# Kernel tuning notes

Hardware: AMD Instinct MI355X
Metric: run time of the kernel (lower is better)

The kernel has to match this reference:

```python
import jax, jax.numpy as jnp
import numpy as np

B, N, H, NH = 1024, 101, 128, 8
HD = H // NH
EPS = 1e-5  # torch LayerNorm default


def _xavier(k, shape):
    fan_in, fan_out = shape
    lim = float(np.sqrt(6.0 / (fan_in + fan_out)))
    return jax.random.uniform(k, shape, jnp.float32, -lim, lim)


def setup_inputs() -> dict:
    key = jax.random.key(0)
    ks = jax.random.split(key, 12)
    return {
        "encoder_inputs": jax.random.normal(ks[0], (B, N, H), jnp.float32),
        "pool": jax.random.normal(ks[1], (B, H), jnp.float32),
        "capacity": jnp.ones((B, 1), jnp.float32),
        "demand": jax.random.uniform(ks[2], (B, N), jnp.float32),
        "fc_w": _xavier(ks[3], (H + 1, H)),      # nn.Linear(hidden+1, hidden, bias=False), stored [in,out]
        "fc1_w": _xavier(ks[4], (H, H)),
        "dec_ln_g": jnp.ones((H,), jnp.float32),
        "dec_ln_b": jnp.zeros((H,), jnp.float32),
        "wq": _xavier(ks[5], (H, H)),             # TransformerAttention q/k/v/out projections
        "wk": _xavier(ks[6], (H, H)),
        "wv": _xavier(ks[7], (H, H)),
        "wo": _xavier(ks[8], (H, H)),
        "kp_w": _xavier(ks[9], (H, H)),           # pointer self.k
        "ptr_ln_g": jnp.ones((H,), jnp.float32),
        "ptr_ln_b": jnp.zeros((H,), jnp.float32),
        "n_steps": 120,
        "T": 1,
        "greedy": 1,
    }


def _ln(x, g, b):
    mu = x.mean(-1, keepdims=True)
    v = ((x - mu) ** 2).mean(-1, keepdims=True)
    return (x - mu) * jax.lax.rsqrt(v + EPS) * g + b


def _forward(encoder_inputs, pool, capacity, demand, fc_w, fc1_w, dec_ln_g, dec_ln_b,
             wq, wk, wv, wo, kp_w, ptr_ln_g, ptr_ln_b, n_steps, T):
    b, n, h = encoder_inputs.shape
    # context projections are loop-invariant -> hoist out of the decode loop
    Kh = (encoder_inputs @ wk).reshape(b, n, NH, HD)
    Vh = (encoder_inputs @ wv).reshape(b, n, NH, HD)
    Kp = encoder_inputs @ kp_w            # [B,N,H] pointer keys
    pool_proc = pool @ fc1_w              # [B,H]
    ar = jnp.arange(n)
    arB = jnp.arange(b)
    inv_sqrt_hd = 1.0 / jnp.sqrt(jnp.float32(HD))
    inv_sqrt_h = 1.0 / jnp.sqrt(jnp.float32(h))

    def step(carry, i):
        mask1, cap, idx, inp = carry
        # decoder input: fc([emb, remaining_cap]) + fc1(pool), LayerNorm
        d = jnp.concatenate([inp, cap], -1) @ fc_w + pool_proc
        d = _ln(d, dec_ln_g, dec_ln_b)
        # ---- update_mask ----
        hit = (ar[None, :] == idx[:, None]) & (idx[:, None] != 0)
        mask1 = jnp.where((i > 0) & hit, 1.0, mask1)
        infeas = (mask1[:, 1:] > 0) | (demand[:, 1:] > cap)      # customers
        any_feas = jnp.any(~infeas, axis=-1)
        depot_m = jnp.where(i == 0, True, (idx == 0) & any_feas)  # mask depot if at depot & feasible cust exists
        all_cust = jnp.all(infeas, axis=-1)
        depot_m = jnp.where(all_cust, False, depot_m)             # only depot allowed if no feasible customer
        mb = jnp.concatenate([depot_m[:, None], infeas], axis=1)  # [B,N] bool, True = masked
        # ---- TransformerAttention (mhalayer) ----
        Qh = (d @ wq).reshape(b, NH, HD)
        logit = jnp.einsum('bhd,bnhd->bhn', Qh, Kh) * inv_sqrt_hd
        logit = jnp.where(mb[:, None, :], -jnp.inf, logit)
        attn = jax.nn.softmax(logit, axis=-1)
        x = jnp.einsum('bhn,bnhd->bhd', attn, Vh).reshape(b, h) @ wo
        # ---- pointer compatibility ----
        xn = _ln(x, ptr_ln_g, ptr_ln_b)
        comp = jnp.einsum('bh,bnh->bn', xn, Kp) * inv_sqrt_h
        comp = jnp.where(mb, -jnp.inf, comp)
        comp = jnp.where(jnp.all(mb, axis=-1, keepdims=True), 0.0, comp)
        p = jax.nn.softmax(comp / T, axis=-1) + 1e-10
        p = p / p.sum(axis=-1, keepdims=True)
        idx = jnp.argmax(p, axis=-1)                              # greedy selection
        lp = jnp.log(jnp.take_along_axis(p, idx[:, None], 1)[:, 0])
        done = mask1[:, 1:].sum(-1) >= (n - 1)
        lp = jnp.where(done, 0.0, lp)
        # ---- update_state (demand lookups via .item() in torch -> stop_gradient) ----
        sel = jax.lax.stop_gradient(jnp.take_along_axis(demand, idx[:, None], 1))
        cap = jnp.where(idx[:, None] == 0, jax.lax.stop_gradient(capacity), cap - sel)
        inp = encoder_inputs[arB, idx]
        return (mask1, cap, idx, inp), (idx, lp)

    init = (jnp.zeros((b, n), jnp.float32), capacity,
            jnp.zeros((b,), jnp.int32), encoder_inputs[:, 0])
    _, (idxs, lps) = jax.lax.scan(step, init, jnp.arange(n_steps))
    last = idxs[-1]
    final = jnp.where(last == 0, -1, 0).astype(jnp.int32)
    actions = jnp.concatenate(
        [jnp.zeros((b, 1), jnp.int32), idxs.T.astype(jnp.int32), final[:, None]], axis=1)
    log_p = lps.sum(0)
    return actions, log_p


def reference(encoder_inputs, pool, capacity, demand, fc_w, fc1_w, dec_ln_g, dec_ln_b,
              wq, wk, wv, wo, kp_w, ptr_ln_g, ptr_ln_b, n_steps, T, greedy):
    # greedy flag: this reference implements the greedy=True path (deterministic argmax).
    return _forward(encoder_inputs, pool, capacity, demand, fc_w, fc1_w, dec_ln_g,
                    dec_ln_b, wq, wk, wv, wo, kp_w, ptr_ln_g, ptr_ln_b,
                    int(n_steps), float(T))
```

## Files before the change

kernel.cpp:

```cpp
#include <hip/hip_runtime.h>
#include <math.h>

constexpr int N_ = 101, H_ = 128;
constexpr float EPS_ = 1e-5f;

constexpr int OFF_QEF = 0;
constexpr int OFF_KT  = 12928;
constexpr int OFF_AT  = 25960;
constexpr int OFF_XV  = 26776;
constexpr int OFF_YR  = 26920;
constexpr int OFF_CP  = 27064;
constexpr int OFF_RS  = 27192;
constexpr int LDS_WORDS = 27512;
constexpr int LDS_BYTES = LDS_WORDS * 4;

__device__ __forceinline__ float rdlane(float v, int l) {
  return __int_as_float(__builtin_amdgcn_readlane(__float_as_int(v), l));
}
template<int CTRL, int RM>
__device__ __forceinline__ float dppadd(float x) {
  int v = __builtin_amdgcn_update_dpp(0, __float_as_int(x), CTRL, RM, 0xf, true);
  return x + __int_as_float(v);
}
template<int CTRL, int RM>
__device__ __forceinline__ float dppmax(float x) {
  int v = __builtin_amdgcn_update_dpp(__float_as_int(x), __float_as_int(x), CTRL, RM, 0xf, false);
  return fmaxf(x, __int_as_float(v));
}
__device__ __forceinline__ float wave_sum(float x) {
  x = dppadd<0x111,0xf>(x); x = dppadd<0x112,0xf>(x);
  x = dppadd<0x114,0xf>(x); x = dppadd<0x118,0xf>(x);
  x = dppadd<0x142,0xa>(x); x = dppadd<0x143,0xc>(x);
  return rdlane(x, 63);
}
__device__ __forceinline__ float wave_max(float x) {
  x = dppmax<0x111,0xf>(x); x = dppmax<0x112,0xf>(x);
  x = dppmax<0x114,0xf>(x); x = dppmax<0x118,0xf>(x);
  x = dppmax<0x142,0xa>(x); x = dppmax<0x143,0xc>(x);
  return rdlane(x, 63);
}
__device__ __forceinline__ float grp4_sum(float x) {
  x = dppadd<0x111,0xf>(x);
  x = dppadd<0x112,0xf>(x);
  return x;
}
__device__ __forceinline__ int swz(int k) { return (k >> 5) * 36 + (k & 31); }

__global__ __launch_bounds__(512, 2) void gat_decoder(
    const float* __restrict__ enc, const float* __restrict__ pool,
    const float* __restrict__ capac, const float* __restrict__ dem,
    const float* __restrict__ fcw, const float* __restrict__ fc1w,
    const float* __restrict__ lng, const float* __restrict__ lnb,
    const float* __restrict__ wq, const float* __restrict__ wk,
    const float* __restrict__ wvm, const float* __restrict__ wo,
    const float* __restrict__ kpw, const float* __restrict__ plg,
    const float* __restrict__ plb, const int* __restrict__ tp,
    float* __restrict__ out, int Bv, int ns)
{
  extern __shared__ float sm[];
  const int tid  = threadIdx.x;
  const int b    = blockIdx.x;
  const int lane = tid & 63;
  const int wvid = tid >> 6;
  const int sl   = lane & 3;
  const int lc   = lane >> 2;
  const int col  = wvid * 16 + lc;
  const int n1 = lane, n2 = lane + 64;

  const float NEG_INF = -__builtin_inff();
  int ti = tp[0];
  float Tf = (ti > 1000000 || ti < -1000000) ? __int_as_float((int)ti) : (float)ti;
  const float inv_sqrt_h = 1.0f / sqrtf(128.0f);
  const float PSUM_CONST = 1.0f + (float)N_ * 1e-10f;

  const float* encb = enc + (size_t)b * (N_ * H_);

  float* QEF = sm + OFF_QEF; float* KT = sm + OFF_KT;
  float* AT = sm + OFF_AT;   float* XVp = sm + OFF_XV;
  float* YRp = sm + OFF_YR;  float* CP = sm + OFF_CP;
  float* RS = sm + OFF_RS;

  const int j3 = tid & 127;
  const int g3 = __builtin_amdgcn_readfirstlane(tid >> 7);
  const int r03 = g3 * 26, nr3 = (g3 == 3) ? 23 : 26;

  {
    const float* pb = pool + (size_t)b * H_;
    float p = 0.f;
    #pragma unroll
    for (int r = 0; r < 32; ++r) p = fmaf(pb[g3 * 32 + r], fc1w[(g3 * 32 + r) * H_ + j3], p);
    AT[g3 * 128 + j3] = p;
  }
  {
    float acc[26];
    #pragma unroll
    for (int t = 0; t < 26; ++t) acc[t] = 0.f;
    for (int k0 = 0; k0 < H_; k0 += 8) {
      float w8[8];
      #pragma unroll
      for (int kk = 0; kk < 8; ++kk) w8[kk] = kpw[(k0 + kk) * H_ + j3];
      #pragma unroll
      for (int t = 0; t < 26; ++t) if (t < nr3) {
        const float* ep = encb + (r03 + t) * H_ + k0;
        #pragma unroll
        for (int kk = 0; kk < 8; ++kk) acc[t] = fmaf(ep[kk], w8[kk], acc[t]);
      }
    }
    #pragma unroll
    for (int t = 0; t < 26; ++t) if (t < nr3) KT[(r03 + t) * 129 + j3] = acc[t];
  }
  __syncthreads();

  if (tid < 128) CP[tid] = AT[tid] + AT[128 + tid] + AT[256 + tid] + AT[384 + tid];
  float kpT[32], kps, cpb;
  {
    const int neff = (col < N_) ? col : (N_ - 1);
    const float* src = KT + neff * 129 + sl * 32;
    float ks = 0.f, cb = 0.f;
    #pragma unroll
    for (int r = 0; r < 32; ++r) {
      const float kv = src[r];
      const float pg = plg[sl * 32 + r];
      const float pb2 = plb[sl * 32 + r];
      ks = fmaf(kv, pg, ks);
      cb = fmaf(kv, pb2, cb);
      kpT[r] = kv * pg;
    }
    kps = grp4_sum(ks); cpb = grp4_sum(cb);
  }
  __syncthreads();

  {
    const float pcj = CP[j3];
    float acc[26];
    #pragma unroll
    for (int t = 0; t < 26; ++t) acc[t] = pcj;
    for (int k0 = 0; k0 < H_; k0 += 8) {
      float w8[8];
      #pragma unroll
      for (int kk = 0; kk < 8; ++kk) w8[kk] = fcw[(k0 + kk) * H_ + j3];
      #pragma unroll
      for (int t = 0; t < 26; ++t) if (t < nr3) {
        const float* ep = encb + (r03 + t) * H_ + k0;
        #pragma unroll
        for (int kk = 0; kk < 8; ++kk) acc[t] = fmaf(ep[kk], w8[kk], acc[t]);
      }
    }
    #pragma unroll
    for (int t = 0; t < 26; ++t) if (t < nr3) KT[(r03 + t) * 129 + j3] = acc[t];
  }
  __syncthreads();

  {
    float qacc[26];
    #pragma unroll
    for (int t = 0; t < 26; ++t) qacc[t] = 0.f;
    for (int k0 = 0; k0 < H_; k0 += 8) {
      float w8[8];
      #pragma unroll
      for (int kk = 0; kk < 8; ++kk) w8[kk] = wq[(k0 + kk) * H_ + j3] * lng[k0 + kk];
      #pragma unroll
      for (int t = 0; t < 26; ++t) if (t < nr3) {
        const float* erow = KT + (r03 + t) * 129 + k0;
        #pragma unroll
        for (int kk = 0; kk < 8; ++kk) qacc[t] = fmaf(erow[kk], w8[kk], qacc[t]);
      }
    }
    #pragma unroll
    for (int t = 0; t < 26; ++t) if (t < nr3) QEF[(r03 + t) * 128 + j3] = qacc[t];
  }
  if (tid < N_) {
    const float* base = KT + tid * 129;
    float s = 0.f, s2 = 0.f, sf = 0.f, fs = 0.f, fs2 = 0.f;
    for (int r = 0; r < 128; ++r) {
      const float v = base[r];
      const float fr = fcw[128 * H_ + r];
      s += v; s2 = fmaf(v, v, s2); sf = fmaf(v, fr, sf);
      fs += fr; fs2 = fmaf(fr, fr, fs2);
    }
    RS[tid] = s; RS[104 + tid] = s2; RS[208 + tid] = sf;
    if (tid == 0) { RS[312] = fs; RS[313] = fs2; }
  }
  __syncthreads();

  {
    float acc[26];
    #pragma unroll
    for (int t = 0; t < 26; ++t) acc[t] = 0.f;
    for (int k0 = 0; k0 < H_; k0 += 8) {
      float w8[8];
      #pragma unroll
      for (int kk = 0; kk < 8; ++kk) w8[kk] = wk[(k0 + kk) * H_ + j3];
      #pragma unroll
      for (int t = 0; t < 26; ++t) if (t < nr3) {
        const float* ep = encb + (r03 + t) * H_ + k0;
        #pragma unroll
        for (int kk = 0; kk < 8; ++kk) acc[t] = fmaf(ep[kk], w8[kk], acc[t]);
      }
    }
    #pragma unroll
    for (int t = 0; t < 26; ++t) if (t < nr3) KT[(r03 + t) * 129 + j3] = acc[t];
  }
  float vh[26];
  {
    const int r0v = sl * 26, nrv = (sl == 3) ? 23 : 26;
    #pragma unroll
    for (int t = 0; t < 26; ++t) vh[t] = 0.f;
    for (int k0 = 0; k0 < H_; k0 += 8) {
      float w8[8];
      #pragma unroll
      for (int kk = 0; kk < 8; ++kk) w8[kk] = wvm[(k0 + kk) * H_ + col];
      #pragma unroll
      for (int t = 0; t < 26; ++t) if (t < nrv) {
        const float* ep = encb + (r0v + t) * H_ + k0;
        #pragma unroll
        for (int kk = 0; kk < 8; ++kk) vh[t] = fmaf(ep[kk], w8[kk], vh[t]);
      }
    }
  }
  float wo_r[32];
  #pragma unroll
  for (int r = 0; r < 32; ++r) wo_r[r] = wo[(sl * 32 + r) * H_ + col];
  float wqs = 0.f, qb = 0.f, wfc = 0.f;
  for (int r = 0; r < 128; ++r) {
    const float w = wq[r * H_ + col];
    const float lg = lng[r], lb = lnb[r], fr = fcw[128 * H_ + r];
    wqs = fmaf(w, lg, wqs);
    qb  = fmaf(w, lb, qb);
    wfc = fmaf(w * lg, fr, wfc);
  }
  const float capv = capac[b];
  float cap = capv, lpsum = 0.f;
  float demA = dem[(size_t)b * N_ + n1];
  float demC = (n2 < N_) ? dem[(size_t)b * N_ + n2] : 0.f;
  int vis = 0, pidx = 0;
  bool m1a = false, m1c = false, mbA, mbB;
  {
    bool infA = (n1 >= 1) && (demA > cap);
    bool infB = (n2 >= N_) || (demC > cap);
    bool feasA = (n1 >= 1) && !infA;
    bool feasB = (n2 < N_) && !infB;
    const bool anyf = __any(feasA || feasB);
    mbA = (n1 == 0) ? anyf : infA;
    mbB = infB;
  }
  __syncthreads();
  const float fcsum = RS[312], fcs2 = RS[313];

  for (int i = 0; i < ns; ++i) {
    const int pu = __builtin_amdgcn_readfirstlane(pidx);

    {
      const float efsum = RS[pu], efs2 = RS[104 + pu], effc = RS[208 + pu];
      const float mu = (efsum + cap * fcsum) * (1.f / 128.f);
      const float msq = (efs2 + 2.f * cap * effc + cap * cap * fcs2) * (1.f / 128.f);
      const float inv = 1.0f / sqrtf(msq - mu * mu + EPS_);
      const float qefv = QEF[pu * 128 + col];
      const float q = inv * (qefv + cap * wfc - mu * wqs) + qb;
      const float* kb1 = KT + n1 * 129 + wvid * 16;
      const float* kb2 = KT + ((n2 < N_) ? n2 : n1) * 129 + wvid * 16;
      float a1 = 0.f, a2r = 0.f;
      #pragma unroll
      for (int d = 0; d < 16; ++d) {
        const float qdv = rdlane(q, 4 * d);
        a1  = fmaf(qdv, kb1[d], a1);
        a2r = fmaf(qdv, kb2[d], a2r);
      }
      a1 = mbA ? NEG_INF : a1 * 0.25f;
      float a2 = (n2 < N_ && !mbB) ? a2r * 0.25f : NEG_INF;
      const float mx = wave_max(fmaxf(a1, a2));
      float e1 = expf(a1 - mx);
      float e2 = (n2 < N_) ? expf(a2 - mx) : 0.f;
      const float ss = wave_sum(e1 + e2);
      AT[wvid * N_ + n1] = e1 / ss;
      if (n2 < N_) AT[wvid * N_ + n2] = e2 / ss;
      const float* aw = AT + wvid * N_ + sl * 26;
      const int nrv = (sl == 3) ? 23 : 26;
      float x = 0.f;
      #pragma unroll
      for (int t = 0; t < 26; ++t) if (t < nrv) x = fmaf(aw[t], vh[t], x);
      x = grp4_sum(x);
      if (sl == 3) XVp[swz(col)] = x;
    }
    __syncthreads();

    {
      const float4* xp4 = (const float4*)(XVp + sl * 36);
      float y = 0.f;
      #pragma unroll
      for (int r4 = 0; r4 < 8; ++r4) {
        const float4 u = xp4[r4];
        y = fmaf(wo_r[r4 * 4 + 0], u.x, y);
        y = fmaf(wo_r[r4 * 4 + 1], u.y, y);
        y = fmaf(wo_r[r4 * 4 + 2], u.z, y);
        y = fmaf(wo_r[r4 * 4 + 3], u.w, y);
      }
      y = grp4_sum(y);
      if (sl == 3) YRp[swz(col)] = y;
    }
    __syncthreads();

    {
      const float YA = YRp[swz(n1)], YC = YRp[swz(n2 & 127)];
      const float mu = wave_sum(YA + YC) * (1.f / 128.f);
      const float da = YA - mu, dc = YC - mu;
      const float inv = 1.0f / sqrtf(wave_sum(da * da + dc * dc) * (1.f / 128.f) + EPS_);
      const float4* yp4 = (const float4*)(YRp + sl * 36);
      float c = 0.f;
      #pragma unroll
      for (int r4 = 0; r4 < 8; ++r4) {
        const float4 u = yp4[r4];
        c = fmaf(kpT[r4 * 4 + 0], u.x, c);
        c = fmaf(kpT[r4 * 4 + 1], u.y, c);
        c = fmaf(kpT[r4 * 4 + 2], u.z, c);
        c = fmaf(kpT[r4 * 4 + 3], u.w, c);
      }
      c = grp4_sum(c);
      const float comp = inv * (c - mu * kps) + cpb;
      if (sl == 3 && col < N_) CP[col] = comp;
    }
    __syncthreads();

    {
      const bool allmb = __all(mbA && mbB);
      float c1 = mbA ? NEG_INF : CP[n1] * inv_sqrt_h / Tf;
      float c2 = (n2 < N_ && !mbB) ? CP[n2 & 127] * inv_sqrt_h / Tf : NEG_INF;
      if (allmb) { c1 = 0.f; c2 = (n2 < N_) ? 0.f : NEG_INF; }
      const float mx = wave_max(fmaxf(c1, c2));
      const unsigned long long b1 = __ballot(c1 == mx);
      const unsigned long long b2 = __ballot(c2 == mx);
      const int bis = b1 ? (__ffsll((long long)b1) - 1)
                         : (64 + __ffsll((long long)b2) - 1);
      float e1 = expf(c1 - mx);
      float e2 = (n2 < N_) ? expf(c2 - mx) : 0.f;
      const float ss = wave_sum(e1 + e2);
      float lp = logf((1.0f / ss + 1e-10f) / PSUM_CONST);
      if (vis >= N_ - 1) lp = 0.f;
      lpsum += lp;
      const float dsel = (bis < 64) ? rdlane(demA, bis) : rdlane(demC, bis - 64);
      cap = (bis == 0) ? capv : (cap - dsel);
      if (bis != 0) {
        const bool newly = ((bis == n1) && !m1a) || ((bis == n2) && !m1c);
        if (__any(newly)) vis += 1;
        m1a = m1a || (bis == n1);
        m1c = m1c || (bis == n2);
      }
      bool infA = (n1 >= 1) && (m1a || demA > cap);
      bool infB = (n2 >= N_) || m1c || (demC > cap);
      bool feasA = (n1 >= 1) && !infA;
      bool feasB = (n2 < N_) && !infB;
      const bool anyf = __any(feasA || feasB);
      const bool depot_m = anyf && (bis == 0);
      mbA = (n1 == 0) ? depot_m : infA;
      mbB = infB;
      pidx = bis;
      if (wvid == 0 && lane == 0) out[(size_t)b * (ns + 2) + 1 + i] = (float)bis;
    }
  }

  if (wvid == 0 && lane == 0) {
    out[(size_t)b * (ns + 2)] = 0.f;
    out[(size_t)b * (ns + 2) + ns + 1] = (pidx == 0) ? -1.f : 0.f;
    out[(size_t)Bv * (ns + 2) + b] = lpsum;
  }
}

extern "C" void kernel_launch(void* const* d_in, const int* in_sizes, int n_in,
                              void* d_out, int out_size, void* d_ws, size_t ws_size,
                              hipStream_t stream) {
  const int Bv = in_sizes[0] / (N_ * H_);
  const int ns = out_size / Bv - 3;
  (void)hipFuncSetAttribute(reinterpret_cast<const void*>(gat_decoder),
                            hipFuncAttributeMaxDynamicSharedMemorySize, LDS_BYTES);
  gat_decoder<<<dim3(Bv), dim3(512), LDS_BYTES, stream>>>(
      (const float*)d_in[0],  (const float*)d_in[1],  (const float*)d_in[2],
      (const float*)d_in[3],  (const float*)d_in[4],  (const float*)d_in[5],
      (const float*)d_in[6],  (const float*)d_in[7],  (const float*)d_in[8],
      (const float*)d_in[9],  (const float*)d_in[10], (const float*)d_in[11],
      (const float*)d_in[12], (const float*)d_in[13], (const float*)d_in[14],
      (const int*)d_in[16],
      (float*)d_out, Bv, ns);
}
```

Measured before the change: 2.911 ms.

## Hold attention keys in registers and share one LDS table to double occupancy

Attention key heads, previously stored in LDS, are now loaded once into per-thread registers (khA/khB) and used from there in the decode loop. The QEF and KT regions are merged into one reused LDS table, with the precompute phases reordered so that table is free in time. That roughly halves LDS use, and the launch bound is raised to 4 blocks per CU with static shared memory. The goal is more resident blocks and no per-step LDS key reads, at the cost of 32 extra registers per thread under a tighter register budget, which may cause spilling.

```diff
diff --git a/kernel.cpp b/kernel.cpp
--- a/kernel.cpp
+++ b/kernel.cpp
@@ -4,15 +4,13 @@
 constexpr int N_ = 101, H_ = 128;
 constexpr float EPS_ = 1e-5f;
 
-constexpr int OFF_QEF = 0;
-constexpr int OFF_KT  = 12928;
-constexpr int OFF_AT  = 25960;
-constexpr int OFF_XV  = 26776;
-constexpr int OFF_YR  = 26920;
-constexpr int OFF_CP  = 27064;
-constexpr int OFF_RS  = 27192;
-constexpr int LDS_WORDS = 27512;
-constexpr int LDS_BYTES = LDS_WORDS * 4;
+constexpr int OFF_TAB = 0;
+constexpr int OFF_AT  = 13032;
+constexpr int OFF_XV  = OFF_AT + 816;
+constexpr int OFF_YR  = OFF_XV + 144;
+constexpr int OFF_CP  = OFF_YR + 144;
+constexpr int OFF_RS  = OFF_CP + 128;
+constexpr int LDS_WORDS = OFF_RS + 320;
 
 __device__ __forceinline__ float rdlane(float v, int l) {
   return __int_as_float(__builtin_amdgcn_readlane(__float_as_int(v), l));
@@ -46,7 +44,7 @@
 }
 __device__ __forceinline__ int swz(int k) { return (k >> 5) * 36 + (k & 31); }
 
-__global__ __launch_bounds__(512, 2) void gat_decoder(
+__global__ __launch_bounds__(512, 4) void gat_decoder(
     const float* __restrict__ enc, const float* __restrict__ pool,
     const float* __restrict__ capac, const float* __restrict__ dem,
     const float* __restrict__ fcw, const float* __restrict__ fc1w,
@@ -57,7 +55,7 @@
     const float* __restrict__ plb, const int* __restrict__ tp,
     float* __restrict__ out, int Bv, int ns)
 {
-  extern __shared__ float sm[];
+  __shared__ float sm[LDS_WORDS];
   const int tid  = threadIdx.x;
   const int b    = blockIdx.x;
   const int lane = tid & 63;
@@ -75,7 +73,7 @@
 
   const float* encb = enc + (size_t)b * (N_ * H_);
 
-  float* QEF = sm + OFF_QEF; float* KT = sm + OFF_KT;
+  float* TAB = sm + OFF_TAB;
   float* AT = sm + OFF_AT;   float* XVp = sm + OFF_XV;
   float* YRp = sm + OFF_YR;  float* CP = sm + OFF_CP;
   float* RS = sm + OFF_RS;
@@ -107,7 +105,7 @@
       }
     }
     #pragma unroll
-    for (int t = 0; t < 26; ++t) if (t < nr3) KT[(r03 + t) * 129 + j3] = acc[t];
+    for (int t = 0; t < 26; ++t) if (t < nr3) TAB[(r03 + t) * 129 + j3] = acc[t];
   }
   __syncthreads();
 
@@ -115,7 +113,7 @@
   float kpT[32], kps, cpb;
   {
     const int neff = (col < N_) ? col : (N_ - 1);
-    const float* src = KT + neff * 129 + sl * 32;
+    const float* src = TAB + neff * 129 + sl * 32;
     float ks = 0.f, cb = 0.f;
     #pragma unroll
     for (int r = 0; r < 32; ++r) {
@@ -131,6 +129,36 @@
   __syncthreads();
 
   {
+    float acc[26];
+    #pragma unroll
+    for (int t = 0; t < 26; ++t) acc[t] = 0.f;
+    for (int k0 = 0; k0 < H_; k0 += 8) {
+      float w8[8];
+      #pragma unroll
+      for (int kk = 0; kk < 8; ++kk) w8[kk] = wk[(k0 + kk) * H_ + j3];
+      #pragma unroll
+      for (int t = 0; t < 26; ++t) if (t < nr3) {
+        const float* ep = encb + (r03 + t) * H_ + k0;
+        #pragma unroll
+        for (int kk = 0; kk < 8; ++kk) acc[t] = fmaf(ep[kk], w8[kk], acc[t]);
+      }
+    }
+    #pragma unroll
+    for (int t = 0; t < 26; ++t) if (t < nr3) TAB[(r03 + t) * 129 + j3] = acc[t];
+  }
+  __syncthreads();
+
+  float khA[16], khB[16];
+  {
+    const int row2 = (n2 < N_) ? n2 : n1;
+    const float* s1 = TAB + n1 * 129 + wvid * 16;
+    const float* s2 = TAB + row2 * 129 + wvid * 16;
+    #pragma unroll
+    for (int d = 0; d < 16; ++d) { khA[d] = s1[d]; khB[d] = s2[d]; }
+  }
+  __syncthreads();
+
+  {
     const float pcj = CP[j3];
     float acc[26];
     #pragma unroll
@@ -147,30 +175,12 @@
       }
     }
     #pragma unroll
-    for (int t = 0; t < 26; ++t) if (t < nr3) KT[(r03 + t) * 129 + j3] = acc[t];
-  }
-  __syncthreads();
-
-  {
-    float qacc[26];
-    #pragma unroll
-    for (int t = 0; t < 26; ++t) qacc[t] = 0.f;
-    for (int k0 = 0; k0 < H_; k0 += 8) {
-      float w8[8];
-      #pragma unroll
-      for (int kk = 0; kk < 8; ++kk) w8[kk] = wq[(k0 + kk) * H_ + j3] * lng[k0 + kk];
-      #pragma unroll
-      for (int t = 0; t < 26; ++t) if (t < nr3) {
-        const float* erow = KT + (r03 + t) * 129 + k0;
-        #pragma unroll
-        for (int kk = 0; kk < 8; ++kk) qacc[t] = fmaf(erow[kk], w8[kk], qacc[t]);
-      }
-    }
-    #pragma unroll
-    for (int t = 0; t < 26; ++t) if (t < nr3) QEF[(r03 + t) * 128 + j3] = qacc[t];
-  }
+    for (int t = 0; t < 26; ++t) if (t < nr3) TAB[(r03 + t) * 129 + j3] = acc[t];
+  }
+  __syncthreads();
+
   if (tid < N_) {
-    const float* base = KT + tid * 129;
+    const float* base = TAB + tid * 129;
     float s = 0.f, s2 = 0.f, sf = 0.f, fs = 0.f, fs2 = 0.f;
     for (int r = 0; r < 128; ++r) {
       const float v = base[r];
@@ -181,26 +191,26 @@
     RS[tid] = s; RS[104 + tid] = s2; RS[208 + tid] = sf;
     if (tid == 0) { RS[312] = fs; RS[313] = fs2; }
   }
-  __syncthreads();
-
-  {
-    float acc[26];
-    #pragma unroll
-    for (int t = 0; t < 26; ++t) acc[t] = 0.f;
-    for (int k0 = 0; k0 < H_; k0 += 8) {
-      float w8[8];
-      #pragma unroll
-      for (int kk = 0; kk < 8; ++kk) w8[kk] = wk[(k0 + kk) * H_ + j3];
+  float qacc[26];
+  {
+    #pragma unroll
+    for (int t = 0; t < 26; ++t) qacc[t] = 0.f;
+    for (int k0 = 0; k0 < H_; k0 += 8) {
+      float w8[8];
+      #pragma unroll
+      for (int kk = 0; kk < 8; ++kk) w8[kk] = wq[(k0 + kk) * H_ + j3] * lng[k0 + kk];
       #pragma unroll
       for (int t = 0; t < 26; ++t) if (t < nr3) {
-        const float* ep = encb + (r03 + t) * H_ + k0;
-        #pragma unroll
-        for (int kk = 0; kk < 8; ++kk) acc[t] = fmaf(ep[kk], w8[kk], acc[t]);
-      }
-    }
-    #pragma unroll
-    for (int t = 0; t < 26; ++t) if (t < nr3) KT[(r03 + t) * 129 + j3] = acc[t];
-  }
+        const float* erow = TAB + (r03 + t) * 129 + k0;
+        #pragma unroll
+        for (int kk = 0; kk < 8; ++kk) qacc[t] = fmaf(erow[kk], w8[kk], qacc[t]);
+      }
+    }
+  }
+  __syncthreads();
+
+  #pragma unroll
+  for (int t = 0; t < 26; ++t) if (t < nr3) TAB[(r03 + t) * 128 + j3] = qacc[t];
   float vh[26];
   {
     const int r0v = sl * 26, nrv = (sl == 3) ? 23 : 26;
@@ -255,16 +265,14 @@
       const float mu = (efsum + cap * fcsum) * (1.f / 128.f);
       const float msq = (efs2 + 2.f * cap * effc + cap * cap * fcs2) * (1.f / 128.f);
       const float inv = 1.0f / sqrtf(msq - mu * mu + EPS_);
-      const float qefv = QEF[pu * 128 + col];
+      const float qefv = TAB[pu * 128 + col];
       const float q = inv * (qefv + cap * wfc - mu * wqs) + qb;
-      const float* kb1 = KT + n1 * 129 + wvid * 16;
-      const float* kb2 = KT + ((n2 < N_) ? n2 : n1) * 129 + wvid * 16;
       float a1 = 0.f, a2r = 0.f;
       #pragma unroll
       for (int d = 0; d < 16; ++d) {
         const float qdv = rdlane(q, 4 * d);
-        a1  = fmaf(qdv, kb1[d], a1);
-        a2r = fmaf(qdv, kb2[d], a2r);
+        a1  = fmaf(qdv, khA[d], a1);
+        a2r = fmaf(qdv, khB[d], a2r);
       }
       a1 = mbA ? NEG_INF : a1 * 0.25f;
       float a2 = (n2 < N_ && !mbB) ? a2r * 0.25f : NEG_INF;
@@ -370,9 +378,7 @@
                               hipStream_t stream) {
   const int Bv = in_sizes[0] / (N_ * H_);
   const int ns = out_size / Bv - 3;
-  (void)hipFuncSetAttribute(reinterpret_cast<const void*>(gat_decoder),
-                            hipFuncAttributeMaxDynamicSharedMemorySize, LDS_BYTES);
-  gat_decoder<<<dim3(Bv), dim3(512), LDS_BYTES, stream>>>(
+  gat_decoder<<<dim3(Bv), dim3(512), 0, stream>>>(
       (const float*)d_in[0],  (const float*)d_in[1],  (const float*)d_in[2],
       (const float*)d_in[3],  (const float*)d_in[4],  (const float*)d_in[5],
       (const float*)d_in[6],  (const float*)d_in[7],  (const float*)d_in[8],
```

New measurement: 4.856 ms. +66.8%, slower.

## Process two batch elements per workgroup to amortize barriers and weight loads

Applied to the files above, without the earlier changes.

Each 512-thread block now decodes two batch items at once, interleaving their per-step attention, projection and pointer phases so they share one set of barriers and the register-resident weight loads. The attention keys are moved from LDS into registers, and LDS regions are duplicated per item. The block count is halved and launch bounds drop to one block per SIMD group, which raises register pressure and lowers occupancy. The launch also assumes an even batch size.

```diff
diff --git a/kernel.cpp b/kernel.cpp
--- a/kernel.cpp
+++ b/kernel.cpp
@@ -4,14 +4,19 @@
 constexpr int N_ = 101, H_ = 128;
 constexpr float EPS_ = 1e-5f;
 
-constexpr int OFF_QEF = 0;
-constexpr int OFF_KT  = 12928;
-constexpr int OFF_AT  = 25960;
-constexpr int OFF_XV  = 26776;
-constexpr int OFF_YR  = 26920;
-constexpr int OFF_CP  = 27064;
-constexpr int OFF_RS  = 27192;
-constexpr int LDS_WORDS = 27512;
+constexpr int OFF_REGA = 0;
+constexpr int OFF_REGB = 13056;
+constexpr int OFF_ATA  = 26112;
+constexpr int OFF_ATB  = 26928;
+constexpr int OFF_XVA  = 27744;
+constexpr int OFF_XVB  = 27888;
+constexpr int OFF_YRA  = 28032;
+constexpr int OFF_YRB  = 28176;
+constexpr int OFF_CPA  = 28320;
+constexpr int OFF_CPB  = 28448;
+constexpr int OFF_RSA  = 28576;
+constexpr int OFF_RSB  = 28896;
+constexpr int LDS_WORDS = 29216;
 constexpr int LDS_BYTES = LDS_WORDS * 4;
 
 __device__ __forceinline__ float rdlane(float v, int l) {
@@ -46,7 +51,68 @@
 }
 __device__ __forceinline__ int swz(int k) { return (k >> 5) * 36 + (k & 31); }
 
-__global__ __launch_bounds__(512, 2) void gat_decoder(
+__device__ __forceinline__ void stage_tab(const float* __restrict__ W,
+                                          const float* __restrict__ ENCB,
+                                          float* __restrict__ REG,
+                                          int j3, int r03, int nr3, float init)
+{
+  float acc[26];
+  #pragma unroll
+  for (int t = 0; t < 26; ++t) acc[t] = init;
+  for (int k0 = 0; k0 < H_; k0 += 8) {
+    float w8[8];
+    #pragma unroll
+    for (int kk = 0; kk < 8; ++kk) w8[kk] = W[(k0 + kk) * H_ + j3];
+    #pragma unroll
+    for (int t = 0; t < 26; ++t) if (t < nr3) {
+      const float* ep = ENCB + (r03 + t) * H_ + k0;
+      #pragma unroll
+      for (int kk = 0; kk < 8; ++kk) acc[t] = fmaf(ep[kk], w8[kk], acc[t]);
+    }
+  }
+  #pragma unroll
+  for (int t = 0; t < 26; ++t) if (t < nr3) REG[(r03 + t) * 129 + j3] = acc[t];
+}
+
+__device__ __forceinline__ void row_stats(const float* __restrict__ REG,
+                                          float* __restrict__ RS,
+                                          const float* __restrict__ fcw, int tid)
+{
+  if (tid < N_) {
+    const float* base = REG + tid * 129;
+    float s = 0.f, s2 = 0.f, sf = 0.f, fs = 0.f, fs2 = 0.f;
+    for (int r = 0; r < 128; ++r) {
+      const float v = base[r];
+      const float fr = fcw[128 * H_ + r];
+      s += v; s2 = fmaf(v, v, s2); sf = fmaf(v, fr, sf);
+      fs += fr; fs2 = fmaf(fr, fr, fs2);
+    }
+    RS[tid] = s; RS[104 + tid] = s2; RS[208 + tid] = sf;
+    if (tid == 0) { RS[312] = fs; RS[313] = fs2; }
+  }
+}
+
+__device__ __forceinline__ void qef_compute(const float* __restrict__ REG,
+                                            const float* __restrict__ wq,
+                                            const float* __restrict__ lng,
+                                            int j3, int r03, int nr3, float (&qacc)[26])
+{
+  #pragma unroll
+  for (int t = 0; t < 26; ++t) qacc[t] = 0.f;
+  for (int k0 = 0; k0 < H_; k0 += 8) {
+    float w8[8];
+    #pragma unroll
+    for (int kk = 0; kk < 8; ++kk) w8[kk] = wq[(k0 + kk) * H_ + j3] * lng[k0 + kk];
+    #pragma unroll
+    for (int t = 0; t < 26; ++t) if (t < nr3) {
+      const float* erow = REG + (r03 + t) * 129 + k0;
+      #pragma unroll
+      for (int kk = 0; kk < 8; ++kk) qacc[t] = fmaf(erow[kk], w8[kk], qacc[t]);
+    }
+  }
+}
+
+__global__ __launch_bounds__(512, 1) void gat_decoder(
     const float* __restrict__ enc, const float* __restrict__ pool,
     const float* __restrict__ capac, const float* __restrict__ dem,
     const float* __restrict__ fcw, const float* __restrict__ fc1w,
@@ -59,162 +125,134 @@
 {
   extern __shared__ float sm[];
   const int tid  = threadIdx.x;
-  const int b    = blockIdx.x;
   const int lane = tid & 63;
   const int wvid = tid >> 6;
   const int sl   = lane & 3;
   const int lc   = lane >> 2;
   const int col  = wvid * 16 + lc;
   const int n1 = lane, n2 = lane + 64;
+  const int b0 = blockIdx.x * 2, b1 = b0 + 1;
 
   const float NEG_INF = -__builtin_inff();
   int ti = tp[0];
   float Tf = (ti > 1000000 || ti < -1000000) ? __int_as_float((int)ti) : (float)ti;
   const float inv_sqrt_h = 1.0f / sqrtf(128.0f);
+  const float sT = inv_sqrt_h / Tf;
   const float PSUM_CONST = 1.0f + (float)N_ * 1e-10f;
 
-  const float* encb = enc + (size_t)b * (N_ * H_);
-
-  float* QEF = sm + OFF_QEF; float* KT = sm + OFF_KT;
-  float* AT = sm + OFF_AT;   float* XVp = sm + OFF_XV;
-  float* YRp = sm + OFF_YR;  float* CP = sm + OFF_CP;
-  float* RS = sm + OFF_RS;
+  const float* encA = enc + (size_t)b0 * (N_ * H_);
+  const float* encB = enc + (size_t)b1 * (N_ * H_);
+
+  float* REG_A = sm + OFF_REGA; float* REG_B = sm + OFF_REGB;
+  float* AT_A = sm + OFF_ATA;   float* AT_B = sm + OFF_ATB;
+  float* XV_A = sm + OFF_XVA;   float* XV_B = sm + OFF_XVB;
+  float* YR_A = sm + OFF_YRA;   float* YR_B = sm + OFF_YRB;
+  float* CP_A = sm + OFF_CPA;   float* CP_B = sm + OFF_CPB;
+  float* RS_A = sm + OFF_RSA;   float* RS_B = sm + OFF_RSB;
 
   const int j3 = tid & 127;
   const int g3 = __builtin_amdgcn_readfirstlane(tid >> 7);
   const int r03 = g3 * 26, nr3 = (g3 == 3) ? 23 : 26;
 
   {
-    const float* pb = pool + (size_t)b * H_;
-    float p = 0.f;
-    #pragma unroll
-    for (int r = 0; r < 32; ++r) p = fmaf(pb[g3 * 32 + r], fc1w[(g3 * 32 + r) * H_ + j3], p);
-    AT[g3 * 128 + j3] = p;
-  }
-  {
-    float acc[26];
-    #pragma unroll
-    for (int t = 0; t < 26; ++t) acc[t] = 0.f;
+    const float* pa = pool + (size_t)b0 * H_;
+    const float* pb = pool + (size_t)b1 * H_;
+    float sa = 0.f, sb = 0.f;
+    #pragma unroll
+    for (int r = 0; r < 32; ++r) {
+      const float w = fc1w[(g3 * 32 + r) * H_ + j3];
+      sa = fmaf(pa[g3 * 32 + r], w, sa);
+      sb = fmaf(pb[g3 * 32 + r], w, sb);
+    }
+    AT_A[g3 * 128 + j3] = sa;
+    AT_B[g3 * 128 + j3] = sb;
+  }
+  __syncthreads();
+  if (tid < 128) {
+    CP_A[tid] = AT_A[tid] + AT_A[128 + tid] + AT_A[256 + tid] + AT_A[384 + tid];
+    CP_B[tid] = AT_B[tid] + AT_B[128 + tid] + AT_B[256 + tid] + AT_B[384 + tid];
+  }
+
+  stage_tab(kpw, encA, REG_A, j3, r03, nr3, 0.f);
+  stage_tab(kpw, encB, REG_B, j3, r03, nr3, 0.f);
+  __syncthreads();
+  float kpT_a[32], kps_a, cpb_a, kpT_b[32], kps_b, cpb_b;
+  {
+    const int neff = (col < N_) ? col : (N_ - 1);
+    const float* sa = REG_A + neff * 129 + sl * 32;
+    const float* sb = REG_B + neff * 129 + sl * 32;
+    float ka = 0.f, ca = 0.f, kb = 0.f, cb = 0.f;
+    #pragma unroll
+    for (int r = 0; r < 32; ++r) {
+      const float pg = plg[sl * 32 + r];
+      const float pl = plb[sl * 32 + r];
+      const float va = sa[r], vb = sb[r];
+      ka = fmaf(va, pg, ka); ca = fmaf(va, pl, ca);
+      kb = fmaf(vb, pg, kb); cb = fmaf(vb, pl, cb);
+      kpT_a[r] = va * pg; kpT_b[r] = vb * pg;
+    }
+    kps_a = grp4_sum(ka); cpb_a = grp4_sum(ca);
+    kps_b = grp4_sum(kb); cpb_b = grp4_sum(cb);
+  }
+  __syncthreads();
+
+  stage_tab(wk, encA, REG_A, j3, r03, nr3, 0.f);
+  stage_tab(wk, encB, REG_B, j3, r03, nr3, 0.f);
+  __syncthreads();
+  float khA_a[16], khB_a[16], khA_b[16], khB_b[16];
+  {
+    const int row2 = (n2 < N_) ? n2 : n1;
+    const float* a1p = REG_A + n1 * 129 + wvid * 16;
+    const float* a2p = REG_A + row2 * 129 + wvid * 16;
+    const float* b1p = REG_B + n1 * 129 + wvid * 16;
+    const float* b2p = REG_B + row2 * 129 + wvid * 16;
+    #pragma unroll
+    for (int d = 0; d < 16; ++d) {
+      khA_a[d] = a1p[d]; khB_a[d] = a2p[d];
+      khA_b[d] = b1p[d]; khB_b[d] = b2p[d];
+    }
+  }
+  __syncthreads();
+
+  stage_tab(fcw, encA, REG_A, j3, r03, nr3, CP_A[j3]);
+  stage_tab(fcw, encB, REG_B, j3, r03, nr3, CP_B[j3]);
+  __syncthreads();
+
+  row_stats(REG_A, RS_A, fcw, tid);
+  {
+    float qacc[26];
+    qef_compute(REG_A, wq, lng, j3, r03, nr3, qacc);
+    __syncthreads();
+    #pragma unroll
+    for (int t = 0; t < 26; ++t) if (t < nr3) REG_A[(r03 + t) * 128 + j3] = qacc[t];
+  }
+  row_stats(REG_B, RS_B, fcw, tid);
+  {
+    float qacc[26];
+    qef_compute(REG_B, wq, lng, j3, r03, nr3, qacc);
+    __syncthreads();
+    #pragma unroll
+    for (int t = 0; t < 26; ++t) if (t < nr3) REG_B[(r03 + t) * 128 + j3] = qacc[t];
+  }
+
+  float vh_a[26], vh_b[26];
+  {
+    const int r0v = sl * 26, nrv = (sl == 3) ? 23 : 26;
+    #pragma unroll
+    for (int t = 0; t < 26; ++t) { vh_a[t] = 0.f; vh_b[t] = 0.f; }
     for (int k0 = 0; k0 < H_; k0 += 8) {
       float w8[8];
       #pragma unroll
-      for (int kk = 0; kk < 8; ++kk) w8[kk] = kpw[(k0 + kk) * H_ + j3];
-      #pragma unroll
-      for (int t = 0; t < 26; ++t) if (t < nr3) {
-        const float* ep = encb + (r03 + t) * H_ + k0;
+      for (int kk = 0; kk < 8; ++kk) w8[kk] = wvm[(k0 + kk) * H_ + col];
+      #pragma unroll
+      for (int t = 0; t < 26; ++t) if (t < nrv) {
+        const float* ea = encA + (r0v + t) * H_ + k0;
+        const float* eb = encB + (r0v + t) * H_ + k0;
         #pragma unroll
-        for (int kk = 0; kk < 8; ++kk) acc[t] = fmaf(ep[kk], w8[kk], acc[t]);
-      }
-    }
-    #pragma unroll
-    for (int t = 0; t < 26; ++t) if (t < nr3) KT[(r03 + t) * 129 + j3] = acc[t];
-  }
-  __syncthreads();
-
-  if (tid < 128) CP[tid] = AT[tid] + AT[128 + tid] + AT[256 + tid] + AT[384 + tid];
-  float kpT[32], kps, cpb;
-  {
-    const int neff = (col < N_) ? col : (N_ - 1);
-    const float* src = KT + neff * 129 + sl * 32;
-    float ks = 0.f, cb = 0.f;
-    #pragma unroll
-    for (int r = 0; r < 32; ++r) {
-      const float kv = src[r];
-      const float pg = plg[sl * 32 + r];
-      const float pb2 = plb[sl * 32 + r];
-      ks = fmaf(kv, pg, ks);
-      cb = fmaf(kv, pb2, cb);
-      kpT[r] = kv * pg;
-    }
-    kps = grp4_sum(ks); cpb = grp4_sum(cb);
-  }
-  __syncthreads();
-
-  {
-    const float pcj = CP[j3];
-    float acc[26];
-    #pragma unroll
-    for (int t = 0; t < 26; ++t) acc[t] = pcj;
-    for (int k0 = 0; k0 < H_; k0 += 8) {
-      float w8[8];
-      #pragma unroll
-      for (int kk = 0; kk < 8; ++kk) w8[kk] = fcw[(k0 + kk) * H_ + j3];
-      #pragma unroll
-      for (int t = 0; t < 26; ++t) if (t < nr3) {
-        const float* ep = encb + (r03 + t) * H_ + k0;
-        #pragma unroll
-        for (int kk = 0; kk < 8; ++kk) acc[t] = fmaf(ep[kk], w8[kk], acc[t]);
-      }
-    }
-    #pragma unroll
-    for (int t = 0; t < 26; ++t) if (t < nr3) KT[(r03 + t) * 129 + j3] = acc[t];
-  }
-  __syncthreads();
-
-  {
-    float qacc[26];
-    #pragma unroll
-    for (int t = 0; t < 26; ++t) qacc[t] = 0.f;
-    for (int k0 = 0; k0 < H_; k0 += 8) {
-      float w8[8];
-      #pragma unroll
-      for (int kk = 0; kk < 8; ++kk) w8[kk] = wq[(k0 + kk) * H_ + j3] * lng[k0 + kk];
-      #pragma unroll
-      for (int t = 0; t < 26; ++t) if (t < nr3) {
-        const float* erow = KT + (r03 + t) * 129 + k0;
-        #pragma unroll
-        for (int kk = 0; kk < 8; ++kk) qacc[t] = fmaf(erow[kk], w8[kk], qacc[t]);
-      }
-    }
-    #pragma unroll
-    for (int t = 0; t < 26; ++t) if (t < nr3) QEF[(r03 + t) * 128 + j3] = qacc[t];
-  }
-  if (tid < N_) {
-    const float* base = KT + tid * 129;
-    float s = 0.f, s2 = 0.f, sf = 0.f, fs = 0.f, fs2 = 0.f;
-    for (int r = 0; r < 128; ++r) {
-      const float v = base[r];
-      const float fr = fcw[128 * H_ + r];
-      s += v; s2 = fmaf(v, v, s2); sf = fmaf(v, fr, sf);
-      fs += fr; fs2 = fmaf(fr, fr, fs2);
-    }
-    RS[tid] = s; RS[104 + tid] = s2; RS[208 + tid] = sf;
-    if (tid == 0) { RS[312] = fs; RS[313] = fs2; }
-  }
-  __syncthreads();
-
-  {
-    float acc[26];
-    #pragma unroll
-    for (int t = 0; t < 26; ++t) acc[t] = 0.f;
-    for (int k0 = 0; k0 < H_; k0 += 8) {
-      float w8[8];
-      #pragma unroll
-      for (int kk = 0; kk < 8; ++kk) w8[kk] = wk[(k0 + kk) * H_ + j3];
-      #pragma unroll
-      for (int t = 0; t < 26; ++t) if (t < nr3) {
-        const float* ep = encb + (r03 + t) * H_ + k0;
-        #pragma unroll
-        for (int kk = 0; kk < 8; ++kk) acc[t] = fmaf(ep[kk], w8[kk], acc[t]);
-      }
-    }
-    #pragma unroll
-    for (int t = 0; t < 26; ++t) if (t < nr3) KT[(r03 + t) * 129 + j3] = acc[t];
-  }
-  float vh[26];
-  {
-    const int r0v = sl * 26, nrv = (sl == 3) ? 23 : 26;
-    #pragma unroll
-    for (int t = 0; t < 26; ++t) vh[t] = 0.f;
-    for (int k0 = 0; k0 < H_; k0 += 8) {
-      float w8[8];
-      #pragma unroll
-      for (int kk = 0; kk < 8; ++kk) w8[kk] = wvm[(k0 + kk) * H_ + col];
-      #pragma unroll
-      for (int t = 0; t < 26; ++t) if (t < nrv) {
-        const float* ep = encb + (r0v + t) * H_ + k0;
-        #pragma unroll
-        for (int kk = 0; kk < 8; ++kk) vh[t] = fmaf(ep[kk], w8[kk], vh[t]);
+        for (int kk = 0; kk < 8; ++kk) {
+          vh_a[t] = fmaf(ea[kk], w8[kk], vh_a[t]);
+          vh_b[t] = fmaf(eb[kk], w8[kk], vh_b[t]);
+        }
       }
     }
   }
@@ -229,139 +267,223 @@
     qb  = fmaf(w, lb, qb);
     wfc = fmaf(w * lg, fr, wfc);
   }
-  const float capv = capac[b];
-  float cap = capv, lpsum = 0.f;
-  float demA = dem[(size_t)b * N_ + n1];
-  float demC = (n2 < N_) ? dem[(size_t)b * N_ + n2] : 0.f;
-  int vis = 0, pidx = 0;
-  bool m1a = false, m1c = false, mbA, mbB;
-  {
-    bool infA = (n1 >= 1) && (demA > cap);
-    bool infB = (n2 >= N_) || (demC > cap);
-    bool feasA = (n1 >= 1) && !infA;
-    bool feasB = (n2 < N_) && !infB;
-    const bool anyf = __any(feasA || feasB);
-    mbA = (n1 == 0) ? anyf : infA;
-    mbB = infB;
-  }
-  __syncthreads();
-  const float fcsum = RS[312], fcs2 = RS[313];
+  const float capv_a = capac[b0], capv_b = capac[b1];
+  float cap_a = capv_a, cap_b = capv_b, lpsum_a = 0.f, lpsum_b = 0.f;
+  float demA_a = dem[(size_t)b0 * N_ + n1];
+  float demC_a = (n2 < N_) ? dem[(size_t)b0 * N_ + n2] : 0.f;
+  float demA_b = dem[(size_t)b1 * N_ + n1];
+  float demC_b = (n2 < N_) ? dem[(size_t)b1 * N_ + n2] : 0.f;
+  int vis_a = 0, pidx_a = 0, vis_b = 0, pidx_b = 0;
+  bool m1a_a = false, m1c_a = false, mbA_a, mbB_a;
+  bool m1a_b = false, m1c_b = false, mbA_b, mbB_b;
+  {
+    bool infA = (n1 >= 1) && (demA_a > cap_a);
+    bool infB = (n2 >= N_) || (demC_a > cap_a);
+    const bool anyf = __any(((n1 >= 1) && !infA) || ((n2 < N_) && !infB));
+    mbA_a = (n1 == 0) ? anyf : infA;
+    mbB_a = infB;
+  }
+  {
+    bool infA = (n1 >= 1) && (demA_b > cap_b);
+    bool infB = (n2 >= N_) || (demC_b > cap_b);
+    const bool anyf = __any(((n1 >= 1) && !infA) || ((n2 < N_) && !infB));
+    mbA_b = (n1 == 0) ? anyf : infA;
+    mbB_b = infB;
+  }
+  __syncthreads();
+  const float fcsum = RS_A[312], fcs2 = RS_A[313];
 
   for (int i = 0; i < ns; ++i) {
-    const int pu = __builtin_amdgcn_readfirstlane(pidx);
-
-    {
-      const float efsum = RS[pu], efs2 = RS[104 + pu], effc = RS[208 + pu];
-      const float mu = (efsum + cap * fcsum) * (1.f / 128.f);
-      const float msq = (efs2 + 2.f * cap * effc + cap * cap * fcs2) * (1.f / 128.f);
+    {
+      const int pu = __builtin_amdgcn_readfirstlane(pidx_a);
+      const float efsum = RS_A[pu], efs2 = RS_A[104 + pu], effc = RS_A[208 + pu];
+      const float mu = (efsum + cap_a * fcsum) * (1.f / 128.f);
+      const float msq = (efs2 + 2.f * cap_a * effc + cap_a * cap_a * fcs2) * (1.f / 128.f);
       const float inv = 1.0f / sqrtf(msq - mu * mu + EPS_);
-      const float qefv = QEF[pu * 128 + col];
-      const float q = inv * (qefv + cap * wfc - mu * wqs) + qb;
-      const float* kb1 = KT + n1 * 129 + wvid * 16;
-      const float* kb2 = KT + ((n2 < N_) ? n2 : n1) * 129 + wvid * 16;
+      const float q = inv * (REG_A[pu * 128 + col] + cap_a * wfc - mu * wqs) + qb;
       float a1 = 0.f, a2r = 0.f;
       #pragma unroll
       for (int d = 0; d < 16; ++d) {
         const float qdv = rdlane(q, 4 * d);
-        a1  = fmaf(qdv, kb1[d], a1);
-        a2r = fmaf(qdv, kb2[d], a2r);
-      }
-      a1 = mbA ? NEG_INF : a1 * 0.25f;
-      float a2 = (n2 < N_ && !mbB) ? a2r * 0.25f : NEG_INF;
+        a1  = fmaf(qdv, khA_a[d], a1);
+        a2r = fmaf(qdv, khB_a[d], a2r);
+      }
+      a1 = mbA_a ? NEG_INF : a1 * 0.25f;
+      float a2 = (n2 < N_ && !mbB_a) ? a2r * 0.25f : NEG_INF;
       const float mx = wave_max(fmaxf(a1, a2));
       float e1 = expf(a1 - mx);
       float e2 = (n2 < N_) ? expf(a2 - mx) : 0.f;
       const float ss = wave_sum(e1 + e2);
-      AT[wvid * N_ + n1] = e1 / ss;
-      if (n2 < N_) AT[wvid * N_ + n2] = e2 / ss;
-      const float* aw = AT + wvid * N_ + sl * 26;
+      AT_A[wvid * N_ + n1] = e1 / ss;
+      if (n2 < N_) AT_A[wvid * N_ + n2] = e2 / ss;
+      const float* aw = AT_A + wvid * N_ + sl * 26;
       const int nrv = (sl == 3) ? 23 : 26;
       float x = 0.f;
       #pragma unroll
-      for (int t = 0; t < 26; ++t) if (t < nrv) x = fmaf(aw[t], vh[t], x);
+      for (int t = 0; t < 26; ++t) if (t < nrv) x = fmaf(aw[t], vh_a[t], x);
       x = grp4_sum(x);
-      if (sl == 3) XVp[swz(col)] = x;
+      if (sl == 3) XV_A[swz(col)] = x;
+    }
+    {
+      const int pu = __builtin_amdgcn_readfirstlane(pidx_b);
+      const float efsum = RS_B[pu], efs2 = RS_B[104 + pu], effc = RS_B[208 + pu];
+      const float mu = (efsum + cap_b * fcsum) * (1.f / 128.f);
+      const float msq = (efs2 + 2.f * cap_b * effc + cap_b * cap_b * fcs2) * (1.f / 128.f);
+      const float inv = 1.0f / sqrtf(msq - mu * mu + EPS_);
+      const float q = inv * (REG_B[pu * 128 + col] + cap_b * wfc - mu * wqs) + qb;
+      float a1 = 0.f, a2r = 0.f;
+      #pragma unroll
+      for (int d = 0; d < 16; ++d) {
+        const float qdv = rdlane(q, 4 * d);
+        a1  = fmaf(qdv, khA_b[d], a1);
+        a2r = fmaf(qdv, khB_b[d], a2r);
+      }
+      a1 = mbA_b ? NEG_INF : a1 * 0.25f;
+      float a2 = (n2 < N_ && !mbB_b) ? a2r * 0.25f : NEG_INF;
+      const float mx = wave_max(fmaxf(a1, a2));
+      float e1 = expf(a1 - mx);
+      float e2 = (n2 < N_) ? expf(a2 - mx) : 0.f;
+      const float ss = wave_sum(e1 + e2);
+      AT_B[wvid * N_ + n1] = e1 / ss;
+      if (n2 < N_) AT_B[wvid * N_ + n2] = e2 / ss;
+      const float* aw = AT_B + wvid * N_ + sl * 26;
+      const int nrv = (sl == 3) ? 23 : 26;
+      float x = 0.f;
+      #pragma unroll
+      for (int t = 0; t < 26; ++t) if (t < nrv) x = fmaf(aw[t], vh_b[t], x);
+      x = grp4_sum(x);
+      if (sl == 3) XV_B[swz(col)] = x;
     }
     __syncthreads();
 
     {
-      const float4* xp4 = (const float4*)(XVp + sl * 36);
-      float y = 0.f;
+      const float4* xa = (const float4*)(XV_A + sl * 36);
+      const float4* xb = (const float4*)(XV_B + sl * 36);
+      float ya = 0.f, yb = 0.f;
       #pragma unroll
       for (int r4 = 0; r4 < 8; ++r4) {
-        const float4 u = xp4[r4];
-        y = fmaf(wo_r[r4 * 4 + 0], u.x, y);
-        y = fmaf(wo_r[r4 * 4 + 1], u.y, y);
-        y = fmaf(wo_r[r4 * 4 + 2], u.z, y);
-        y = fmaf(wo_r[r4 * 4 + 3], u.w, y);
-      }
-      y = grp4_sum(y);
-      if (sl == 3) YRp[swz(col)] = y;
+        const float4 ua = xa[r4], ub = xb[r4];
+        ya = fmaf(wo_r[r4*4+0], ua.x, ya); yb = fmaf(wo_r[r4*4+0], ub.x, yb);
+        ya = fmaf(wo_r[r4*4+1], ua.y, ya); yb = fmaf(wo_r[r4*4+1], ub.y, yb);
+        ya = fmaf(wo_r[r4*4+2], ua.z, ya); yb = fmaf(wo_r[r4*4+2], ub.z, yb);
+        ya = fmaf(wo_r[r4*4+3], ua.w, ya); yb = fmaf(wo_r[r4*4+3], ub.w, yb);
+      }
+      ya = grp4_sum(ya); yb = grp4_sum(yb);
+      if (sl == 3) { YR_A[swz(col)] = ya; YR_B[swz(col)] = yb; }
     }
     __syncthreads();
 
     {
-      const float YA = YRp[swz(n1)], YC = YRp[swz(n2 & 127)];
+      const float YA = YR_A[swz(n1)], YC = YR_A[swz(n2 & 127)];
       const float mu = wave_sum(YA + YC) * (1.f / 128.f);
       const float da = YA - mu, dc = YC - mu;
       const float inv = 1.0f / sqrtf(wave_sum(da * da + dc * dc) * (1.f / 128.f) + EPS_);
-      const float4* yp4 = (const float4*)(YRp + sl * 36);
+      const float4* yp4 = (const float4*)(YR_A + sl * 36);
       float c = 0.f;
       #pragma unroll
       for (int r4 = 0; r4 < 8; ++r4) {
         const float4 u = yp4[r4];
-        c = fmaf(kpT[r4 * 4 + 0], u.x, c);
-        c = fmaf(kpT[r4 * 4 + 1], u.y, c);
-        c = fmaf(kpT[r4 * 4 + 2], u.z, c);
-        c = fmaf(kpT[r4 * 4 + 3], u.w, c);
+        c = fmaf(kpT_a[r4*4+0], u.x, c);
+        c = fmaf(kpT_a[r4*4+1], u.y, c);
+        c = fmaf(kpT_a[r4*4+2], u.z, c);
+        c = fmaf(kpT_a[r4*4+3], u.w, c);
       }
       c = grp4_sum(c);
-      const float comp = inv * (c - mu * kps) + cpb;
-      if (sl == 3 && col < N_) CP[col] = comp;
+      const float comp = inv * (c - mu * kps_a) + cpb_a;
+      if (sl == 3 && col < N_) CP_A[col] = comp;
+    }
+    {
+      const float YA = YR_B[swz(n1)], YC = YR_B[swz(n2 & 127)];
+      const float mu = wave_sum(YA + YC) * (1.f / 128.f);
+      const float da = YA - mu, dc = YC - mu;
+      const float inv = 1.0f / sqrtf(wave_sum(da * da + dc * dc) * (1.f / 128.f) + EPS_);
+      const float4* yp4 = (const float4*)(YR_B + sl * 36);
+      float c = 0.f;
+      #pragma unroll
+      for (int r4 = 0; r4 < 8; ++r4) {
+        const float4 u = yp4[r4];
+        c = fmaf(kpT_b[r4*4+0], u.x, c);
+        c = fmaf(kpT_b[r4*4+1], u.y, c);
+        c = fmaf(kpT_b[r4*4+2], u.z, c);
+        c = fmaf(kpT_b[r4*4+3], u.w, c);
+      }
+      c = grp4_sum(c);
+      const float comp = inv * (c - mu * kps_b) + cpb_b;
+      if (sl == 3 && col < N_) CP_B[col] = comp;
     }
     __syncthreads();
 
     {
-      const bool allmb = __all(mbA && mbB);
-      float c1 = mbA ? NEG_INF : CP[n1] * inv_sqrt_h / Tf;
-      float c2 = (n2 < N_ && !mbB) ? CP[n2 & 127] * inv_sqrt_h / Tf : NEG_INF;
+      const bool allmb = __all(mbA_a && mbB_a);
+      float c1 = mbA_a ? NEG_INF : CP_A[n1] * sT;
+      float c2 = (n2 < N_ && !mbB_a) ? CP_A[n2 & 127] * sT : NEG_INF;
       if (allmb) { c1 = 0.f; c2 = (n2 < N_) ? 0.f : NEG_INF; }
       const float mx = wave_max(fmaxf(c1, c2));
-      const unsigned long long b1 = __ballot(c1 == mx);
-      const unsigned long long b2 = __ballot(c2 == mx);
-      const int bis = b1 ? (__ffsll((long long)b1) - 1)
-                         : (64 + __ffsll((long long)b2) - 1);
+      const unsigned long long q1 = __ballot(c1 == mx);
+      const unsigned long long q2 = __ballot(c2 == mx);
+      const int bis = q1 ? (__ffsll((long long)q1) - 1) : (64 + __ffsll((long long)q2) - 1);
       float e1 = expf(c1 - mx);
       float e2 = (n2 < N_) ? expf(c2 - mx) : 0.f;
       const float ss = wave_sum(e1 + e2);
       float lp = logf((1.0f / ss + 1e-10f) / PSUM_CONST);
-      if (vis >= N_ - 1) lp = 0.f;
-      lpsum += lp;
-      const float dsel = (bis < 64) ? rdlane(demA, bis) : rdlane(demC, bis - 64);
-      cap = (bis == 0) ? capv : (cap - dsel);
+      if (vis_a >= N_ - 1) lp = 0.f;
+      lpsum_a += lp;
+      const float dsel = (bis < 64) ? rdlane(demA_a, bis) : rdlane(demC_a, bis - 64);
+      cap_a = (bis == 0) ? capv_a : (cap_a - dsel);
       if (bis != 0) {
-        const bool newly = ((bis == n1) && !m1a) || ((bis == n2) && !m1c);
-        if (__any(newly)) vis += 1;
-        m1a = m1a || (bis == n1);
-        m1c = m1c || (bis == n2);
-      }
-      bool infA = (n1 >= 1) && (m1a || demA > cap);
-      bool infB = (n2 >= N_) || m1c || (demC > cap);
-      bool feasA = (n1 >= 1) && !infA;
-      bool feasB = (n2 < N_) && !infB;
-      const bool anyf = __any(feasA || feasB);
-      const bool depot_m = anyf && (bis == 0);
-      mbA = (n1 == 0) ? depot_m : infA;
-      mbB = infB;
-      pidx = bis;
-      if (wvid == 0 && lane == 0) out[(size_t)b * (ns + 2) + 1 + i] = (float)bis;
+        const bool newly = ((bis == n1) && !m1a_a) || ((bis == n2) && !m1c_a);
+        if (__any(newly)) vis_a += 1;
+        m1a_a = m1a_a || (bis == n1);
+        m1c_a = m1c_a || (bis == n2);
+      }
+      bool infA = (n1 >= 1) && (m1a_a || demA_a > cap_a);
+      bool infB = (n2 >= N_) || m1c_a || (demC_a > cap_a);
+      const bool anyf = __any(((n1 >= 1) && !infA) || ((n2 < N_) && !infB));
+      mbA_a = (n1 == 0) ? (anyf && (bis == 0)) : infA;
+      mbB_a = infB;
+      pidx_a = bis;
+      if (wvid == 0 && lane == 0) out[(size_t)b0 * (ns + 2) + 1 + i] = (float)bis;
+    }
+    {
+      const bool allmb = __all(mbA_b && mbB_b);
+      float c1 = mbA_b ? NEG_INF : CP_B[n1] * sT;
+      float c2 = (n2 < N_ && !mbB_b) ? CP_B[n2 & 127] * sT : NEG_INF;
+      if (allmb) { c1 = 0.f; c2 = (n2 < N_) ? 0.f : NEG_INF; }
+      const float mx = wave_max(fmaxf(c1, c2));
+      const unsigned long long q1 = __ballot(c1 == mx);
+      const unsigned long long q2 = __ballot(c2 == mx);
+      const int bis = q1 ? (__ffsll((long long)q1) - 1) : (64 + __ffsll((long long)q2) - 1);
+      float e1 = expf(c1 - mx);
+      float e2 = (n2 < N_) ? expf(c2 - mx) : 0.f;
+      const float ss = wave_sum(e1 + e2);
+      float lp = logf((1.0f / ss + 1e-10f) / PSUM_CONST);
+      if (vis_b >= N_ - 1) lp = 0.f;
+      lpsum_b += lp;
+      const float dsel = (bis < 64) ? rdlane(demA_b, bis) : rdlane(demC_b, bis - 64);
+      cap_b = (bis == 0) ? capv_b : (cap_b - dsel);
+      if (bis != 0) {
+        const bool newly = ((bis == n1) && !m1a_b) || ((bis == n2) && !m1c_b);
+        if (__any(newly)) vis_b += 1;
+        m1a_b = m1a_b || (bis == n1);
+        m1c_b = m1c_b || (bis == n2);
+      }
+      bool infA = (n1 >= 1) && (m1a_b || demA_b > cap_b);
+      bool infB = (n2 >= N_) || m1c_b || (demC_b > cap_b);
+      const bool anyf = __any(((n1 >= 1) && !infA) || ((n2 < N_) && !infB));
+      mbA_b = (n1 == 0) ? (anyf && (bis == 0)) : infA;
+      mbB_b = infB;
+      pidx_b = bis;
+      if (wvid == 0 && lane == 0) out[(size_t)b1 * (ns + 2) + 1 + i] = (float)bis;
     }
   }
 
   if (wvid == 0 && lane == 0) {
-    out[(size_t)b * (ns + 2)] = 0.f;
-    out[(size_t)b * (ns + 2) + ns + 1] = (pidx == 0) ? -1.f : 0.f;
-    out[(size_t)Bv * (ns + 2) + b] = lpsum;
+    out[(size_t)b0 * (ns + 2)] = 0.f;
+    out[(size_t)b0 * (ns + 2) + ns + 1] = (pidx_a == 0) ? -1.f : 0.f;
+    out[(size_t)Bv * (ns + 2) + b0] = lpsum_a;
+    out[(size_t)b1 * (ns + 2)] = 0.f;
+    out[(size_t)b1 * (ns + 2) + ns + 1] = (pidx_b == 0) ? -1.f : 0.f;
+    out[(size_t)Bv * (ns + 2) + b1] = lpsum_b;
   }
 }
 
@@ -372,7 +494,7 @@
   const int ns = out_size / Bv - 3;
   (void)hipFuncSetAttribute(reinterpret_cast<const void*>(gat_decoder),
                             hipFuncAttributeMaxDynamicSharedMemorySize, LDS_BYTES);
-  gat_decoder<<<dim3(Bv), dim3(512), LDS_BYTES, stream>>>(
+  gat_decoder<<<dim3(Bv / 2), dim3(512), LDS_BYTES, stream>>>(
       (const float*)d_in[0],  (const float*)d_in[1],  (const float*)d_in[2],
       (const float*)d_in[3],  (const float*)d_in[4],  (const float*)d_in[5],
       (const float*)d_in[6],  (const float*)d_in[7],  (const float*)d_in[8],
```

Measured after the change: 4.800 ms. 1.65x slower.
